# Kernel tuning notes

Hardware: AMD Instinct MI355X
Metric: run time of the kernel (lower is better)

The kernel has to match this reference:

```python
import jax, jax.numpy as jnp
import numpy as np

B, S, H, HD = 2, 2048, 16, 128
HID = H * HD            # 2048
FF = 4 * HID            # 8192
ROT = int(HD * 0.25)    # 32 rotary dims (rotary_pct=0.25)
EPS = 1e-5
ROPE_BASE = 10000.0


def _layernorm(x, g, b):
    mu = jnp.mean(x, axis=-1, keepdims=True)
    var = jnp.mean(jnp.square(x - mu), axis=-1, keepdims=True)
    return (x - mu) * jax.lax.rsqrt(var + EPS) * g + b


def _rope_cos_sin(seq_len, dim, dtype):
    inv_freq = 1.0 / (ROPE_BASE ** (np.arange(0, dim, 2, dtype=np.float32) / dim))
    t = np.arange(seq_len, dtype=np.float32)
    freqs = np.outer(t, inv_freq)              # [S, dim/2]
    emb = np.concatenate([freqs, freqs], -1)   # [S, dim]
    return jnp.asarray(np.cos(emb), dtype), jnp.asarray(np.sin(emb), dtype)


def _apply_rope(x, cos, sin):
    # x: [B, H, S, ROT]; GPTNeoX rotate_half
    half = x.shape[-1] // 2
    x1, x2 = x[..., :half], x[..., half:]
    rot = jnp.concatenate([-x2, x1], axis=-1)
    return x * cos[None, None, :, :] + rot * sin[None, None, :, :]


def setup_inputs() -> dict:
    key = jax.random.key(0)
    ks = jax.random.split(key, 8)
    f = jnp.float32
    return {
        "hidden_states": jax.random.normal(ks[0], (B, S, HID), f),
        "ln1_g": jnp.ones((HID,), f), "ln1_b": jnp.zeros((HID,), f),
        "ln2_g": jnp.ones((HID,), f), "ln2_b": jnp.zeros((HID,), f),
        "W_qkv": jax.random.normal(ks[1], (HID, 3 * HID), f) * 0.02,
        "b_qkv": jnp.zeros((3 * HID,), f),
        "W_o": jax.random.normal(ks[2], (HID, HID), f) * 0.02,
        "b_o": jnp.zeros((HID,), f),
        "W_fc": jax.random.normal(ks[3], (HID, FF), f) * 0.02,
        "b_fc": jnp.zeros((FF,), f),
        "W_proj": jax.random.normal(ks[4], (FF, HID), f) * 0.02,
        "b_proj": jnp.zeros((HID,), f),
    }


def reference(hidden_states, ln1_g, ln1_b, ln2_g, ln2_b,
              W_qkv, b_qkv, W_o, b_o, W_fc, b_fc, W_proj, b_proj):
    dtype = hidden_states.dtype
    x = _layernorm(hidden_states, ln1_g, ln1_b)

    # fused QKV, GPTNeoX per-head interleaved layout [B,S,H,3*HD]
    qkv = (x @ W_qkv + b_qkv).reshape(B, S, H, 3 * HD)
    q = jnp.transpose(qkv[..., :HD], (0, 2, 1, 3))          # [B,H,S,HD]
    k = jnp.transpose(qkv[..., HD:2 * HD], (0, 2, 1, 3))
    v = jnp.transpose(qkv[..., 2 * HD:], (0, 2, 1, 3))

    cos, sin = _rope_cos_sin(S, ROT, dtype)
    q = jnp.concatenate([_apply_rope(q[..., :ROT], cos, sin), q[..., ROT:]], -1)
    k = jnp.concatenate([_apply_rope(k[..., :ROT], cos, sin), k[..., ROT:]], -1)

    # eager attention: scores / sqrt(hd), causal mask-fill, softmax, matmul
    scale = 1.0 / jnp.sqrt(jnp.asarray(HD, dtype))
    scores = jnp.einsum("bhqd,bhkd->bhqk", q, k) * scale
    causal = jnp.tril(jnp.ones((S, S), bool))
    scores = jnp.where(causal, scores, jnp.finfo(dtype).min)
    weights = jax.nn.softmax(scores, axis=-1)
    ctx = jnp.einsum("bhqk,bhkd->bhqd", weights, v)          # [B,H,S,HD]
    ctx = jnp.transpose(ctx, (0, 2, 1, 3)).reshape(B, S, HID)
    attn_out = ctx @ W_o + b_o

    # parallel residual: mlp(ln2(h)) + attn(ln1(h)) + h
    m = _layernorm(hidden_states, ln2_g, ln2_b)
    mlp_out = jax.nn.gelu(m @ W_fc + b_fc, approximate=False) @ W_proj + b_proj
    return mlp_out + attn_out + hidden_states
```

## Files before the change

### kernel.cpp

```cpp
#include <hip/hip_runtime.h>
#include <hip/hip_bf16.h>
#include <math.h>

#define BDIM 2
#define SDIM 2048
#define HDIM 16
#define HD 128
#define HID 2048
#define FFD 8192
#define NTOK (BDIM*SDIM)
#define QKVW (3*HID)

typedef __hip_bfloat16 bf16;
typedef __attribute__((ext_vector_type(8))) short short8;
typedef __attribute__((ext_vector_type(4))) short short4_;
typedef __attribute__((ext_vector_type(4))) float floatx4;

__device__ inline short bfbits(float f) {
  bf16 h = __float2bfloat16(f);
  short s;
  __builtin_memcpy(&s, &h, 2);
  return s;
}

__global__ __launch_bounds__(256) void transpose_cvt(
    const float* __restrict__ W, bf16* __restrict__ Wt, int K, int N)
{
  __shared__ float tile[32][33];
  int n0 = blockIdx.x * 32, k0 = blockIdx.y * 32;
  int tx = threadIdx.x, ty = threadIdx.y;
  #pragma unroll
  for (int r = ty; r < 32; r += 8)
    tile[r][tx] = W[(size_t)(k0 + r) * N + n0 + tx];
  __syncthreads();
  #pragma unroll
  for (int r = ty; r < 32; r += 8)
    Wt[(size_t)(n0 + r) * K + k0 + tx] = __float2bfloat16(tile[tx][r]);
}

__global__ __launch_bounds__(256) void ln_both(
    const float* __restrict__ x,
    const float* __restrict__ g1, const float* __restrict__ b1,
    const float* __restrict__ g2, const float* __restrict__ b2,
    bf16* __restrict__ o1, bf16* __restrict__ o2)
{
  int row = blockIdx.x;
  int tid = threadIdx.x;
  const float4* xr = (const float4*)(x + (size_t)row * HID);
  float4 va = xr[tid], vb = xr[tid + 256];
  float s = va.x + va.y + va.z + va.w + vb.x + vb.y + vb.z + vb.w;
  float q = va.x*va.x + va.y*va.y + va.z*va.z + va.w*va.w
          + vb.x*vb.x + vb.y*vb.y + vb.z*vb.z + vb.w*vb.w;
  #pragma unroll
  for (int off = 1; off < 64; off <<= 1) {
    s += __shfl_xor(s, off);
    q += __shfl_xor(q, off);
  }
  __shared__ float red[8];
  int wave = tid >> 6;
  if ((tid & 63) == 0) { red[wave] = s; red[4 + wave] = q; }
  __syncthreads();
  s = red[0] + red[1] + red[2] + red[3];
  q = red[4] + red[5] + red[6] + red[7];
  float mu = s * (1.0f / HID);
  float var = q * (1.0f / HID) - mu * mu;
  float rs = rsqrtf(var + 1e-5f);

  const float4* g1v = (const float4*)g1; const float4* b1v = (const float4*)b1;
  const float4* g2v = (const float4*)g2; const float4* b2v = (const float4*)b2;
  short4_* o1v = (short4_*)(o1 + (size_t)row * HID);
  short4_* o2v = (short4_*)(o2 + (size_t)row * HID);
  #pragma unroll
  for (int p = 0; p < 2; ++p) {
    int e = tid + p * 256;
    float4 xv = (p == 0) ? va : vb;
    float4 gv = g1v[e], bv = b1v[e];
    short4_ pk;
    pk[0] = bfbits((xv.x - mu) * rs * gv.x + bv.x);
    pk[1] = bfbits((xv.y - mu) * rs * gv.y + bv.y);
    pk[2] = bfbits((xv.z - mu) * rs * gv.z + bv.z);
    pk[3] = bfbits((xv.w - mu) * rs * gv.w + bv.w);
    o1v[e] = pk;
    gv = g2v[e]; bv = b2v[e];
    pk[0] = bfbits((xv.x - mu) * rs * gv.x + bv.x);
    pk[1] = bfbits((xv.y - mu) * rs * gv.y + bv.y);
    pk[2] = bfbits((xv.z - mu) * rs * gv.z + bv.z);
    pk[3] = bfbits((xv.w - mu) * rs * gv.w + bv.w);
    o2v[e] = pk;
  }
}

template<int EPI>
__global__ __launch_bounds__(256) void gemm_bt(
    const bf16* __restrict__ A, const bf16* __restrict__ Bt,
    const float* __restrict__ bias,
    float* __restrict__ Cf, bf16* __restrict__ Cb,
    const bf16* __restrict__ r1b, const float* __restrict__ r2,
    int M, int N, int K)
{
  __shared__ bf16 As[128 * 32];
  __shared__ bf16 Bs[128 * 32];
  const int tid = threadIdx.x;
  const int wave = tid >> 6, lane = tid & 63;
  const int quad = lane >> 4, l16 = lane & 15;
  const int n0 = blockIdx.x * 128, m0 = blockIdx.y * 128;
  const int wm = (wave >> 1) * 64, wn = (wave & 1) * 64;
  const int lrow = lane >> 2, lcol = (lane & 3) * 8;

  floatx4 acc[4][4];
  #pragma unroll
  for (int i = 0; i < 4; ++i)
    #pragma unroll
    for (int j = 0; j < 4; ++j) acc[i][j] = (floatx4)0.0f;

  const int KT = K >> 5;
  for (int kt = 0; kt < KT; ++kt) {
    #pragma unroll
    for (int t = 0; t < 2; ++t) {
      int c = wave * 2 + t;
      const bf16* ga = A + (size_t)(m0 + c * 16 + lrow) * K + kt * 32 + lcol;
      const bf16* gb = Bt + (size_t)(n0 + c * 16 + lrow) * K + kt * 32 + lcol;
      __builtin_amdgcn_global_load_lds(
          (const __attribute__((address_space(1))) void*)ga,
          (__attribute__((address_space(3))) void*)&As[c * 512], 16, 0, 0);
      __builtin_amdgcn_global_load_lds(
          (const __attribute__((address_space(1))) void*)gb,
          (__attribute__((address_space(3))) void*)&Bs[c * 512], 16, 0, 0);
    }
    __syncthreads();
    short8 av[4], bv[4];
    #pragma unroll
    for (int i = 0; i < 4; ++i)
      av[i] = *(const short8*)&As[(wm + i * 16 + l16) * 32 + quad * 8];
    #pragma unroll
    for (int j = 0; j < 4; ++j)
      bv[j] = *(const short8*)&Bs[(wn + j * 16 + l16) * 32 + quad * 8];
    #pragma unroll
    for (int i = 0; i < 4; ++i)
      #pragma unroll
      for (int j = 0; j < 4; ++j)
        acc[i][j] = __builtin_amdgcn_mfma_f32_16x16x32_bf16(av[i], bv[j], acc[i][j], 0, 0, 0);
    __syncthreads();
  }

  #pragma unroll
  for (int i = 0; i < 4; ++i) {
    #pragma unroll
    for (int j = 0; j < 4; ++j) {
      int col = n0 + wn + j * 16 + l16;
      float bsv = bias[col];
      #pragma unroll
      for (int r = 0; r < 4; ++r) {
        int row = m0 + wm + i * 16 + quad * 4 + r;
        size_t idx = (size_t)row * N + col;
        float v = acc[i][j][r] + bsv;
        if (EPI == 1) {
          v = 0.5f * v * (1.0f + erff(v * 0.70710678118654752f));
          Cb[idx] = __float2bfloat16(v);
        } else if (EPI == 2) {
          Cf[idx] = v + __bfloat162float(r1b[idx]) + r2[idx];
        } else {
          Cb[idx] = __float2bfloat16(v);
        }
      }
    }
  }
}

__global__ __launch_bounds__(256) void rope_vt(
    bf16* __restrict__ qkv, bf16* __restrict__ vT)
{
  int bh = blockIdx.x, s0 = blockIdx.y * 32;
  int b = bh >> 4, h = bh & 15;
  int tid = threadIdx.x;
  __shared__ bf16 vs[32][136];
  const float qsc = 0.12751740f;

  for (int idx = tid; idx < 512; idx += 256) {
    int sl = idx >> 4, d = idx & 15;
    int s = s0 + sl;
    bf16* base = qkv + (size_t)(b * SDIM + s) * QKVW + h * 384;
    float fr = (float)s * expf(-(float)d * 0.5756462732485114f);
    float c = cosf(fr), sn = sinf(fr);
    float q1 = __bfloat162float(base[d]);
    float q2 = __bfloat162float(base[d + 16]);
    float k1 = __bfloat162float(base[128 + d]);
    float k2 = __bfloat162float(base[128 + d + 16]);
    base[d]        = __float2bfloat16(qsc * (q1 * c - q2 * sn));
    base[d + 16]   = __float2bfloat16(qsc * (q2 * c + q1 * sn));
    base[128 + d]      = __float2bfloat16(k1 * c - k2 * sn);
    base[128 + d + 16] = __float2bfloat16(k2 * c + k1 * sn);
  }
  for (int idx = tid; idx < 32 * 96; idx += 256) {
    int sl = idx / 96, d = 32 + idx % 96;
    bf16* base = qkv + (size_t)(b * SDIM + s0 + sl) * QKVW + h * 384;
    base[d] = __float2bfloat16(qsc * __bfloat162float(base[d]));
  }

  for (int idx = tid; idx < 32 * 128; idx += 256) {
    int sl = idx >> 7, d = idx & 127;
    vs[sl][d] = qkv[(size_t)(b * SDIM + s0 + sl) * QKVW + h * 384 + 256 + d];
  }
  __syncthreads();
  for (int idx = tid; idx < 32 * 128; idx += 256) {
    int d = idx >> 5, sl = idx & 31;
    vT[((size_t)bh * HD + d) * SDIM + s0 + sl] = vs[sl][d];
  }
}

#define LOAD_K(KB, K0) { \
  int krow_ = (K0); \
  _Pragma("unroll") for (int nh_ = 0; nh_ < 2; ++nh_) \
    _Pragma("unroll") for (int c_ = 0; c_ < 4; ++c_) \
      KB[nh_*4+c_] = *(const short8*)&Kb[(size_t)(krow_ + nh_*16 + l16) * QKVW + c_*32 + quad*8]; }

#define SOFTMAX(S0, S1, MR, LR, OO, ROWQ, DOMASK, K0, SLOT) { \
  if (DOMASK) { \
    _Pragma("unroll") for (int r_ = 0; r_ < 4; ++r_) { \
      int row_ = (ROWQ) + quad*4 + r_; \
      S0[r_] = ((K0) + l16 <= row_) ? S0[r_] : -1e30f; \
      S1[r_] = ((K0) + 16 + l16 <= row_) ? S1[r_] : -1e30f; } } \
  _Pragma("unroll") for (int r_ = 0; r_ < 4; ++r_) { \
    float mx_ = fmaxf(S0[r_], S1[r_]); \
    mx_ = fmaxf(mx_, __shfl_xor(mx_, 1)); \
    mx_ = fmaxf(mx_, __shfl_xor(mx_, 2)); \
    mx_ = fmaxf(mx_, __shfl_xor(mx_, 4)); \
    mx_ = fmaxf(mx_, __shfl_xor(mx_, 8)); \
    float mnew_ = fmaxf(MR[r_], mx_); \
    float alpha_ = __builtin_amdgcn_exp2f(MR[r_] - mnew_); \
    MR[r_] = mnew_; \
    S0[r_] = __builtin_amdgcn_exp2f(S0[r_] - mnew_); \
    S1[r_] = __builtin_amdgcn_exp2f(S1[r_] - mnew_); \
    float sm_ = S0[r_] + S1[r_]; \
    sm_ += __shfl_xor(sm_, 1); sm_ += __shfl_xor(sm_, 2); \
    sm_ += __shfl_xor(sm_, 4); sm_ += __shfl_xor(sm_, 8); \
    LR[r_] = LR[r_] * alpha_ + sm_; \
    _Pragma("unroll") for (int d_ = 0; d_ < 8; ++d_) OO[d_][r_] *= alpha_; \
    Ps[wave][SLOT][quad*4 + r_][l16]      = __float2bfloat16(S0[r_]); \
    Ps[wave][SLOT][quad*4 + r_][16 + l16] = __float2bfloat16(S1[r_]); } }

#define FLASH_ITER(IT, KC, KN) { \
  const int k0_ = (IT) * 32; \
  const int k0n_ = ((IT) + 1 < nk) ? k0_ + 32 : 0; \
  LOAD_K(KN, k0n_); \
  short8 vbuf_[8]; \
  _Pragma("unroll") for (int d_ = 0; d_ < 8; ++d_) \
    vbuf_[d_] = *(const short8*)&Vb[(size_t)(d_*16 + l16) * SDIM + k0_ + quad*8]; \
  floatx4 scB_[2]; scB_[0] = (floatx4)0.0f; scB_[1] = (floatx4)0.0f; \
  _Pragma("unroll") for (int c_ = 0; c_ < 4; ++c_) { \
    scB_[0] = __builtin_amdgcn_mfma_f32_16x16x32_bf16(aqB[c_], KC[c_],   scB_[0], 0,0,0); \
    scB_[1] = __builtin_amdgcn_mfma_f32_16x16x32_bf16(aqB[c_], KC[4+c_], scB_[1], 0,0,0); } \
  const bool actA_ = (k0_ <= qa + 15); \
  floatx4 scA_[2]; scA_[0] = (floatx4)0.0f; scA_[1] = (floatx4)0.0f; \
  if (actA_) { \
    _Pragma("unroll") for (int c_ = 0; c_ < 4; ++c_) { \
      scA_[0] = __builtin_amdgcn_mfma_f32_16x16x32_bf16(aqA[c_], KC[c_],   scA_[0], 0,0,0); \
      scA_[1] = __builtin_amdgcn_mfma_f32_16x16x32_bf16(aqA[c_], KC[4+c_], scA_[1], 0,0,0); } } \
  SOFTMAX(scB_[0], scB_[1], mB, lB, oB, qb, (k0_ + 32 >= kmax), k0_, 0); \
  if (actA_) { \
    SOFTMAX(scA_[0], scA_[1], mA, lA, oA, qa, (k0_ + 32 > qa + 15), k0_, 1); \
    short8 pfB_ = *(const short8*)&Ps[wave][0][l16][quad*8]; \
    short8 pfA_ = *(const short8*)&Ps[wave][1][l16][quad*8]; \
    _Pragma("unroll") for (int d_ = 0; d_ < 8; ++d_) { \
      oB[d_] = __builtin_amdgcn_mfma_f32_16x16x32_bf16(pfB_, vbuf_[d_], oB[d_], 0,0,0); \
      oA[d_] = __builtin_amdgcn_mfma_f32_16x16x32_bf16(pfA_, vbuf_[d_], oA[d_], 0,0,0); } \
  } else { \
    short8 pfB_ = *(const short8*)&Ps[wave][0][l16][quad*8]; \
    _Pragma("unroll") for (int d_ = 0; d_ < 8; ++d_) \
      oB[d_] = __builtin_amdgcn_mfma_f32_16x16x32_bf16(pfB_, vbuf_[d_], oB[d_], 0,0,0); } }

__global__ __launch_bounds__(256) void flash_attn(
    const bf16* __restrict__ qkv, const bf16* __restrict__ vT,
    bf16* __restrict__ ctx)
{
  int bh = blockIdx.x;
  int b = bh >> 4, h = bh & 15;
  int tid = threadIdx.x;
  int wave = tid >> 6, lane = tid & 63;
  int quad = lane >> 4, l16 = lane & 15;
  int p = blockIdx.y * 4 + wave;
  int qa = 16 * p;
  int qb = SDIM - 16 * (p + 1);
  int kmax = qb + 16;
  int nk = (kmax + 31) >> 5;
  const bf16* Qb = qkv + (size_t)b * SDIM * QKVW + h * 384;
  const bf16* Kb = Qb + 128;
  const bf16* Vb = vT + (size_t)bh * HD * SDIM;
  __shared__ bf16 Ps[4][2][16][32];

  short8 aqA[4], aqB[4];
  #pragma unroll
  for (int c = 0; c < 4; ++c) {
    aqA[c] = *(const short8*)&Qb[(size_t)(qa + l16) * QKVW + c * 32 + quad * 8];
    aqB[c] = *(const short8*)&Qb[(size_t)(qb + l16) * QKVW + c * 32 + quad * 8];
  }

  floatx4 oA[8], oB[8];
  #pragma unroll
  for (int d = 0; d < 8; ++d) { oA[d] = (floatx4)0.0f; oB[d] = (floatx4)0.0f; }
  float mA[4] = {-INFINITY, -INFINITY, -INFINITY, -INFINITY};
  float mB[4] = {-INFINITY, -INFINITY, -INFINITY, -INFINITY};
  float lA[4] = {0.0f, 0.0f, 0.0f, 0.0f};
  float lB[4] = {0.0f, 0.0f, 0.0f, 0.0f};

  short8 kb0[8], kb1[8];
  LOAD_K(kb0, 0);
  for (int it = 0; it < nk; it += 2) {
    FLASH_ITER(it, kb0, kb1);
    if (it + 1 < nk) { FLASH_ITER(it + 1, kb1, kb0); }
  }

  float rlA[4], rlB[4];
  #pragma unroll
  for (int r = 0; r < 4; ++r) { rlA[r] = 1.0f / lA[r]; rlB[r] = 1.0f / lB[r]; }
  #pragma unroll
  for (int d = 0; d < 8; ++d) {
    #pragma unroll
    for (int r = 0; r < 4; ++r) {
      int rowA = qa + quad * 4 + r;
      int rowB = qb + quad * 4 + r;
      ctx[((size_t)b * SDIM + rowA) * HID + h * HD + d * 16 + l16] =
          __float2bfloat16(oA[d][r] * rlA[r]);
      ctx[((size_t)b * SDIM + rowB) * HID + h * HD + d * 16 + l16] =
          __float2bfloat16(oB[d][r] * rlB[r]);
    }
  }
}

extern "C" void kernel_launch(void* const* d_in, const int* in_sizes, int n_in,
                              void* d_out, int out_size, void* d_ws, size_t ws_size,
                              hipStream_t stream) {
  const float* hidden = (const float*)d_in[0];
  const float* ln1g = (const float*)d_in[1];
  const float* ln1b = (const float*)d_in[2];
  const float* ln2g = (const float*)d_in[3];
  const float* ln2b = (const float*)d_in[4];
  const float* Wqkv = (const float*)d_in[5];
  const float* bqkv = (const float*)d_in[6];
  const float* Wo   = (const float*)d_in[7];
  const float* bo   = (const float*)d_in[8];
  const float* Wfc  = (const float*)d_in[9];
  const float* bfc  = (const float*)d_in[10];
  const float* Wproj= (const float*)d_in[11];
  const float* bproj= (const float*)d_in[12];

  char* ws = (char*)d_ws;
  const size_t SZ_WQKV = (size_t)QKVW * HID * 2;
  const size_t SZ_WO   = (size_t)HID * HID * 2;
  const size_t SZ_WFC  = (size_t)FFD * HID * 2;
  const size_t SZ_WPROJ= (size_t)HID * FFD * 2;
  const size_t SZ_ACT  = (size_t)NTOK * HID * 2;
  const size_t SZ_QKV  = (size_t)NTOK * QKVW * 2;

  bf16* wqkvT = (bf16*)(ws + 0);
  bf16* woT   = (bf16*)(ws + SZ_WQKV);
  bf16* wfcT  = (bf16*)(ws + SZ_WQKV + SZ_WO);
  bf16* wprojT= (bf16*)(ws + SZ_WQKV + SZ_WO + SZ_WFC);
  char* actbase = ws + SZ_WQKV + SZ_WO + SZ_WFC + SZ_WPROJ;
  bf16* xln   = (bf16*)(actbase);
  bf16* mln   = (bf16*)(actbase + SZ_ACT);
  bf16* qkvb  = (bf16*)(actbase + 2 * SZ_ACT);
  bf16* vT    = (bf16*)(actbase + 2 * SZ_ACT + SZ_QKV);
  bf16* ctx   = xln;
  bf16* attnb = wqkvT;
  bf16* hfc   = qkvb;

  dim3 tblk(32, 8);
  transpose_cvt<<<dim3(QKVW / 32, HID / 32), tblk, 0, stream>>>(Wqkv, wqkvT, HID, QKVW);
  transpose_cvt<<<dim3(HID / 32, HID / 32), tblk, 0, stream>>>(Wo, woT, HID, HID);
  transpose_cvt<<<dim3(FFD / 32, HID / 32), tblk, 0, stream>>>(Wfc, wfcT, HID, FFD);
  transpose_cvt<<<dim3(HID / 32, FFD / 32), tblk, 0, stream>>>(Wproj, wprojT, FFD, HID);

  ln_both<<<NTOK, 256, 0, stream>>>(hidden, ln1g, ln1b, ln2g, ln2b, xln, mln);

  gemm_bt<3><<<dim3(48, 32), 256, 0, stream>>>(xln, wqkvT, bqkv, nullptr, qkvb,
                                               nullptr, nullptr, NTOK, QKVW, HID);

  rope_vt<<<dim3(32, SDIM / 32), 256, 0, stream>>>(qkvb, vT);

  flash_attn<<<dim3(32, SDIM / 128), 256, 0, stream>>>(qkvb, vT, ctx);

  gemm_bt<3><<<dim3(16, 32), 256, 0, stream>>>(ctx, woT, bo, nullptr, attnb,
                                               nullptr, nullptr, NTOK, HID, HID);

  gemm_bt<1><<<dim3(64, 32), 256, 0, stream>>>(mln, wfcT, bfc, nullptr, hfc,
                                               nullptr, nullptr, NTOK, FFD, HID);

  gemm_bt<2><<<dim3(16, 32), 256, 0, stream>>>(hfc, wprojT, bproj, (float*)d_out, nullptr,
                                               attnb, hidden, NTOK, HID, FFD);
}
```

Before: 1.093 ms.

## Replace GEMM with 256x256 tile, 8-wave, 4-stage pipelined LDS kernel

Replaces the 128x128 single-buffered GEMM with a 256x256 tile kernel using 8 waves, a 4-deep LDS ring buffer with global_load_lds prefetch three iterations ahead, and XOR-swizzled LDS addressing. It interleaves half-tile MFMA phases with staging, raises wave priority during MFMA, and remaps workgroups with a grid swizzle for cache locality. The aim is to hide global-load latency and cut LDS bank conflicts and per-iteration barriers. LDS use grows to 128KB per block, and the 2048-wide GEMMs now launch only 128 blocks, which may underfill the GPU.

```diff
diff --git a/kernel.cpp b/kernel.cpp
--- a/kernel.cpp
+++ b/kernel.cpp
@@ -91,67 +91,123 @@
 }
 
 template<int EPI>
-__global__ __launch_bounds__(256) void gemm_bt(
+__global__ __launch_bounds__(512, 2) void gemm8(
     const bf16* __restrict__ A, const bf16* __restrict__ Bt,
     const float* __restrict__ bias,
     float* __restrict__ Cf, bf16* __restrict__ Cb,
     const bf16* __restrict__ r1b, const float* __restrict__ r2,
     int M, int N, int K)
 {
-  __shared__ bf16 As[128 * 32];
-  __shared__ bf16 Bs[128 * 32];
+  __shared__ bf16 SA[4][256 * 32];
+  __shared__ bf16 SB[4][256 * 32];
   const int tid = threadIdx.x;
   const int wave = tid >> 6, lane = tid & 63;
   const int quad = lane >> 4, l16 = lane & 15;
-  const int n0 = blockIdx.x * 128, m0 = blockIdx.y * 128;
-  const int wm = (wave >> 1) * 64, wn = (wave & 1) * 64;
-  const int lrow = lane >> 2, lcol = (lane & 3) * 8;
-
-  floatx4 acc[4][4];
-  #pragma unroll
-  for (int i = 0; i < 4; ++i)
+  const int wr = wave >> 2, wc = wave & 3;
+
+  const int nwg = gridDim.x * gridDim.y;
+  const int flat = blockIdx.y * gridDim.x + blockIdx.x;
+  const int swz = (flat & 7) * (nwg >> 3) + (flat >> 3);
+  const int bx = swz % gridDim.x, by = swz / gridDim.x;
+  const int n0 = bx * 256, m0 = by * 256;
+
+  const int stg_r = wave * 16 + (lane >> 2);
+  const int stg_c8 = (((lane & 3) ^ ((lane >> 3) & 3)) << 3);
+  const bf16* stgA = A + (size_t)(m0 + stg_r) * K + stg_c8;
+  const bf16* stgB = Bt + (size_t)(n0 + stg_r) * K + stg_c8;
+  const int ldsOff = wave * 16 * 32;
+
+  const int rd_sw = ((quad ^ ((l16 >> 1) & 3)) << 3);
+  const int rdA = (wr * 128 + l16) * 32 + rd_sw;
+  const int rdB = (wc * 64 + l16) * 32 + rd_sw;
+
+  floatx4 acc[8][4];
+  #pragma unroll
+  for (int i = 0; i < 8; ++i)
     #pragma unroll
     for (int j = 0; j < 4; ++j) acc[i][j] = (floatx4)0.0f;
 
   const int KT = K >> 5;
+
+#define STAGE_A8(KT3) { const int b_ = (KT3) & 3;                              \
+  __builtin_amdgcn_global_load_lds(                                            \
+      (const __attribute__((address_space(1))) void*)(stgA + (size_t)(KT3)*32),\
+      (__attribute__((address_space(3))) void*)&SA[b_][ldsOff], 16, 0, 0);     \
+  __builtin_amdgcn_global_load_lds(                                            \
+      (const __attribute__((address_space(1))) void*)(stgA + (size_t)128*K + (size_t)(KT3)*32), \
+      (__attribute__((address_space(3))) void*)&SA[b_][128*32 + ldsOff], 16, 0, 0); }
+#define STAGE_B8(KT3) { const int b_ = (KT3) & 3;                              \
+  __builtin_amdgcn_global_load_lds(                                            \
+      (const __attribute__((address_space(1))) void*)(stgB + (size_t)(KT3)*32),\
+      (__attribute__((address_space(3))) void*)&SB[b_][ldsOff], 16, 0, 0);     \
+  __builtin_amdgcn_global_load_lds(                                            \
+      (const __attribute__((address_space(1))) void*)(stgB + (size_t)128*K + (size_t)(KT3)*32), \
+      (__attribute__((address_space(3))) void*)&SB[b_][128*32 + ldsOff], 16, 0, 0); }
+
+  STAGE_A8(0); STAGE_B8(0);
+  STAGE_A8(1); STAGE_B8(1);
+  STAGE_A8(2); STAGE_B8(2);
+  asm volatile("s_waitcnt vmcnt(8)" ::: "memory");
+  __builtin_amdgcn_s_barrier();
+
+  short8 av[4], bv[4];
   for (int kt = 0; kt < KT; ++kt) {
-    #pragma unroll
-    for (int t = 0; t < 2; ++t) {
-      int c = wave * 2 + t;
-      const bf16* ga = A + (size_t)(m0 + c * 16 + lrow) * K + kt * 32 + lcol;
-      const bf16* gb = Bt + (size_t)(n0 + c * 16 + lrow) * K + kt * 32 + lcol;
-      __builtin_amdgcn_global_load_lds(
-          (const __attribute__((address_space(1))) void*)ga,
-          (__attribute__((address_space(3))) void*)&As[c * 512], 16, 0, 0);
-      __builtin_amdgcn_global_load_lds(
-          (const __attribute__((address_space(1))) void*)gb,
-          (__attribute__((address_space(3))) void*)&Bs[c * 512], 16, 0, 0);
-    }
-    __syncthreads();
-    short8 av[4], bv[4];
-    #pragma unroll
-    for (int i = 0; i < 4; ++i)
-      av[i] = *(const short8*)&As[(wm + i * 16 + l16) * 32 + quad * 8];
-    #pragma unroll
-    for (int j = 0; j < 4; ++j)
-      bv[j] = *(const short8*)&Bs[(wn + j * 16 + l16) * 32 + quad * 8];
+    const bf16* as_ = &SA[kt & 3][0];
+    const bf16* bs_ = &SB[kt & 3][0];
+    const bool st = (kt + 3) < KT;
+
+    #pragma unroll
+    for (int i = 0; i < 4; ++i) av[i] = *(const short8*)&as_[rdA + i * 512];
+    #pragma unroll
+    for (int j = 0; j < 4; ++j) bv[j] = *(const short8*)&bs_[rdB + j * 512];
+    if (st) STAGE_A8(kt + 3);
+    __builtin_amdgcn_s_barrier();
+    asm volatile("s_waitcnt lgkmcnt(0)" ::: "memory");
+    __builtin_amdgcn_sched_barrier(0);
+    __builtin_amdgcn_s_setprio(1);
     #pragma unroll
     for (int i = 0; i < 4; ++i)
       #pragma unroll
       for (int j = 0; j < 4; ++j)
         acc[i][j] = __builtin_amdgcn_mfma_f32_16x16x32_bf16(av[i], bv[j], acc[i][j], 0, 0, 0);
-    __syncthreads();
-  }
-
-  #pragma unroll
-  for (int i = 0; i < 4; ++i) {
+    __builtin_amdgcn_s_setprio(0);
+    __builtin_amdgcn_s_barrier();
+
+    #pragma unroll
+    for (int i = 0; i < 4; ++i) av[i] = *(const short8*)&as_[rdA + 2048 + i * 512];
+    if (st) STAGE_B8(kt + 3);
+    __builtin_amdgcn_s_barrier();
+    asm volatile("s_waitcnt lgkmcnt(0)" ::: "memory");
+    __builtin_amdgcn_sched_barrier(0);
+    __builtin_amdgcn_s_setprio(1);
+    #pragma unroll
+    for (int i = 0; i < 4; ++i)
+      #pragma unroll
+      for (int j = 0; j < 4; ++j)
+        acc[4 + i][j] = __builtin_amdgcn_mfma_f32_16x16x32_bf16(av[i], bv[j], acc[4 + i][j], 0, 0, 0);
+    __builtin_amdgcn_s_setprio(0);
+
+    if (st) {
+      asm volatile("s_waitcnt vmcnt(8)" ::: "memory");
+    } else if (kt + 3 == KT) {
+      asm volatile("s_waitcnt vmcnt(4)" ::: "memory");
+    } else if (kt + 2 == KT) {
+      asm volatile("s_waitcnt vmcnt(0)" ::: "memory");
+    }
+    if (kt + 1 < KT) __builtin_amdgcn_s_barrier();
+  }
+#undef STAGE_A8
+#undef STAGE_B8
+
+  #pragma unroll
+  for (int i = 0; i < 8; ++i) {
     #pragma unroll
     for (int j = 0; j < 4; ++j) {
-      int col = n0 + wn + j * 16 + l16;
+      int col = n0 + wc * 64 + j * 16 + l16;
       float bsv = bias[col];
       #pragma unroll
       for (int r = 0; r < 4; ++r) {
-        int row = m0 + wm + i * 16 + quad * 4 + r;
+        int row = m0 + wr * 128 + i * 16 + quad * 4 + r;
         size_t idx = (size_t)row * N + col;
         float v = acc[i][j][r] + bsv;
         if (EPI == 1) {
@@ -373,19 +429,19 @@
 
   ln_both<<<NTOK, 256, 0, stream>>>(hidden, ln1g, ln1b, ln2g, ln2b, xln, mln);
 
-  gemm_bt<3><<<dim3(48, 32), 256, 0, stream>>>(xln, wqkvT, bqkv, nullptr, qkvb,
-                                               nullptr, nullptr, NTOK, QKVW, HID);
+  gemm8<3><<<dim3(QKVW / 256, NTOK / 256), 512, 0, stream>>>(
+      xln, wqkvT, bqkv, nullptr, qkvb, nullptr, nullptr, NTOK, QKVW, HID);
 
   rope_vt<<<dim3(32, SDIM / 32), 256, 0, stream>>>(qkvb, vT);
 
   flash_attn<<<dim3(32, SDIM / 128), 256, 0, stream>>>(qkvb, vT, ctx);
 
-  gemm_bt<3><<<dim3(16, 32), 256, 0, stream>>>(ctx, woT, bo, nullptr, attnb,
-                                               nullptr, nullptr, NTOK, HID, HID);
-
-  gemm_bt<1><<<dim3(64, 32), 256, 0, stream>>>(mln, wfcT, bfc, nullptr, hfc,
-                                               nullptr, nullptr, NTOK, FFD, HID);
-
-  gemm_bt<2><<<dim3(16, 32), 256, 0, stream>>>(hfc, wprojT, bproj, (float*)d_out, nullptr,
-                                               attnb, hidden, NTOK, HID, FFD);
-}
+  gemm8<3><<<dim3(HID / 256, NTOK / 256), 512, 0, stream>>>(
+      ctx, woT, bo, nullptr, attnb, nullptr, nullptr, NTOK, HID, HID);
+
+  gemm8<1><<<dim3(FFD / 256, NTOK / 256), 512, 0, stream>>>(
+      mln, wfcT, bfc, nullptr, hfc, nullptr, nullptr, NTOK, FFD, HID);
+
+  gemm8<2><<<dim3(HID / 256, NTOK / 256), 512, 0, stream>>>(
+      hfc, wprojT, bproj, (float*)d_out, nullptr, attnb, hidden, NTOK, HID, FFD);
+}
```

New measurement: 1.120 ms. 1.02x slower.
